# Optimization experiments

Hardware: AMD Instinct MI355X
Metric: run time of the kernel (lower is better)

The kernel has to match this reference:

```python
import jax, jax.numpy as jnp
import numpy as np

BSZ, SEQ, HID = 8, 4096, 1024
N_EXPERTS = 8
CAPACITY = 512  # expert_capacity_per_batch; effective cap = min(SEQ, CAPACITY)
SCALE = 1.0     # routed_scaling_factor


def setup_inputs() -> dict:
    key = jax.random.key(0)
    k1, k2 = jax.random.split(key)
    hidden_states = jax.random.normal(k1, (BSZ, SEQ, HID), dtype=jnp.float32)
    # kaiming_uniform_(a=sqrt(5)) on [d,e] -> bound = 1/sqrt(fan_in=d)
    bound = 1.0 / np.sqrt(HID)
    weight = jax.random.uniform(k2, (HID, N_EXPERTS), dtype=jnp.float32,
                                minval=-bound, maxval=bound)
    return {"hidden_states": hidden_states, "weight": weight}


def reference(hidden_states, weight):
    bsz, seq_len, h = hidden_states.shape
    # gating logits in fp32: [b, s, e]
    logits = jnp.einsum('bsd,de->bse', hidden_states.astype(jnp.float32),
                        weight.astype(jnp.float32))
    affinity = jax.nn.softmax(logits, axis=-1)          # [b, s, e]
    affinity = jnp.transpose(affinity, (0, 2, 1))       # [b, e, s]
    cap = min(seq_len, CAPACITY)                        # static
    # Each expert picks its top-`cap` tokens (sorted descending, like torch.topk)
    topk_scores, topk_indices = jax.lax.top_k(affinity, cap)  # [b, e, cap]
    topk_scores = topk_scores * SCALE
    # dense dispatch mask [b, e, cap, s]: one-hot over token positions
    dispatch_mask = jax.nn.one_hot(topk_indices, seq_len, dtype=jnp.float32)
    return topk_indices, topk_scores, dispatch_mask
```

## Files before the change

kernel.cpp:

```cpp
#include <hip/hip_runtime.h>

constexpr int BSZ = 8, SEQ = 4096, HID = 1024, NE = 8, CAP = 512;
constexpr int ROWS = BSZ * NE;
constexpr size_t IDX_ELEMS = (size_t)ROWS * CAP;
constexpr size_t SCR_OFF = IDX_ELEMS;
constexpr size_t MASK_OFF = IDX_ELEMS * 2;
constexpr size_t MASK_ELEMS = (size_t)ROWS * CAP * SEQ;
constexpr size_t AFF_ELEMS = (size_t)ROWS * SEQ;

typedef float f4v __attribute__((ext_vector_type(4)));

__global__ __launch_bounds__(128) void gating_kernel(const float* __restrict__ hidden,
                                                     const float* __restrict__ weight,
                                                     float* __restrict__ aff)
{
    __shared__ float hls[16][68];
    __shared__ float wls[8][68];
    __shared__ float lls[16][8];

    const int tid = threadIdx.x;
    const int T0 = blockIdx.x * 16;
    const int t = tid >> 3;
    const int e = tid & 7;

    float v0 = 0.f, v1 = 0.f, v2 = 0.f, v3 = 0.f;
    for (int c = 0; c < 16; ++c) {
        __syncthreads();
#pragma unroll
        for (int k = 0; k < 2; ++k) {
            const int j = tid + k * 128;
            const int tt = j >> 4, q = j & 15;
            const float4 v = *(const float4*)(hidden + (size_t)(T0 + tt) * HID + c * 64 + 4 * q);
            *(float4*)&hls[tt][4 * q] = v;
        }
#pragma unroll
        for (int k = 0; k < 4; ++k) {
            const int j = tid + k * 128;
            const int dd = j >> 3, ee = j & 7;
            wls[ee][dd] = weight[(size_t)(c * 64 + dd) * NE + ee];
        }
        __syncthreads();
#pragma unroll
        for (int k = 0; k < 4; ++k) {
            const int base = 16 * k;
            const float4 hA = *(const float4*)&hls[t][base + 0];
            const float4 hB = *(const float4*)&hls[t][base + 4];
            const float4 hC = *(const float4*)&hls[t][base + 8];
            const float4 hD = *(const float4*)&hls[t][base + 12];
            const float4 wA = *(const float4*)&wls[e][base + 0];
            const float4 wB = *(const float4*)&wls[e][base + 4];
            const float4 wC = *(const float4*)&wls[e][base + 8];
            const float4 wD = *(const float4*)&wls[e][base + 12];
            v0 = __fadd_rn(__fmul_rn(hA.x, wA.x),
                 __fadd_rn(__fmul_rn(hB.x, wB.x),
                 __fadd_rn(__fmul_rn(hC.x, wC.x),
                 __fadd_rn(__fmul_rn(hD.x, wD.x), v0))));
            v1 = __fadd_rn(__fmul_rn(hA.y, wA.y),
                 __fadd_rn(__fmul_rn(hB.y, wB.y),
                 __fadd_rn(__fmul_rn(hC.y, wC.y),
                 __fadd_rn(__fmul_rn(hD.y, wD.y), v1))));
            v2 = __fadd_rn(__fmul_rn(hA.z, wA.z),
                 __fadd_rn(__fmul_rn(hB.z, wB.z),
                 __fadd_rn(__fmul_rn(hC.z, wC.z),
                 __fadd_rn(__fmul_rn(hD.z, wD.z), v2))));
            v3 = __fadd_rn(__fmul_rn(hA.w, wA.w),
                 __fadd_rn(__fmul_rn(hB.w, wB.w),
                 __fadd_rn(__fmul_rn(hC.w, wC.w),
                 __fadd_rn(__fmul_rn(hD.w, wD.w), v3))));
        }
    }
    const float logit = __fadd_rn(__fadd_rn(v0, v1), __fadd_rn(v2, v3));

    lls[t][e] = logit;
    __syncthreads();

    float l[8];
#pragma unroll
    for (int k = 0; k < 8; ++k) l[k] = lls[t][k];
    float m = l[0];
#pragma unroll
    for (int k = 1; k < 8; ++k) m = fmaxf(m, l[k]);
    float p[8];
#pragma unroll
    for (int k = 0; k < 8; ++k)
        p[k] = (float)exp((double)__fsub_rn(l[k], m));
    const float s = __fadd_rn(__fadd_rn(__fadd_rn(p[0], p[1]), __fadd_rn(p[2], p[3])),
                              __fadd_rn(__fadd_rn(p[4], p[5]), __fadd_rn(p[6], p[7])));
    const float a = __fdiv_rn(p[e], s);

    const int token = T0 + t;
    const int b = token >> 12;
    const int sidx = token & (SEQ - 1);
    aff[((size_t)b * NE + e) * SEQ + sidx] = a;
}

__global__ __launch_bounds__(1024) void topk_zero_kernel(const float* __restrict__ aff,
                                                         float* __restrict__ out,
                                                         long long zero_elems)
{
    __shared__ unsigned long long keys[SEQ];
    if (blockIdx.x < (unsigned)ROWS) {
        const int row = blockIdx.x;
        const float* a = aff + (size_t)row * SEQ;
        for (int i = threadIdx.x; i < SEQ; i += 1024) {
            const unsigned int fb = __float_as_uint(a[i]);
            keys[i] = ((unsigned long long)fb << 32) | (unsigned int)(SEQ - 1 - i);
        }
        for (int len = 2; len <= SEQ; len <<= 1) {
            for (int stride = len >> 1; stride > 0; stride >>= 1) {
                __syncthreads();
                for (int t = threadIdx.x; t < SEQ / 2; t += 1024) {
                    const int i = (t << 1) - (t & (stride - 1));
                    const int j = i + stride;
                    const unsigned long long ki = keys[i], kj = keys[j];
                    const bool desc = ((i & len) == 0);
                    if (desc ? (ki < kj) : (ki > kj)) { keys[i] = kj; keys[j] = ki; }
                }
            }
        }
        __syncthreads();
        if (threadIdx.x < CAP) {
            const int t = threadIdx.x;
            const unsigned long long k = keys[t];
            const int idx = (SEQ - 1) - (int)(unsigned int)(k & 0xffffffffu);
            out[(size_t)row * CAP + t] = (float)idx;
            out[SCR_OFF + (size_t)row * CAP + t] =
                __uint_as_float((unsigned int)(k >> 32));
        }
    } else {
        const long long nz4 = zero_elems >> 2;
        f4v* mz = (f4v*)(out + MASK_OFF);
        const f4v z4 = {0.f, 0.f, 0.f, 0.f};
        const long long stride = (long long)(gridDim.x - ROWS) * 1024;
        for (long long i = (long long)(blockIdx.x - ROWS) * 1024 + threadIdx.x;
             i < nz4; i += stride)
            __builtin_nontemporal_store(z4, mz + i);
    }
}

__global__ void tailzero_kernel(float* __restrict__ out)
{
    const long long n4 = (long long)(AFF_ELEMS >> 2);
    f4v* mz = (f4v*)(out + MASK_OFF + MASK_ELEMS - AFF_ELEMS);
    const f4v z4 = {0.f, 0.f, 0.f, 0.f};
    const long long i = (long long)blockIdx.x * blockDim.x + threadIdx.x;
    if (i < n4) __builtin_nontemporal_store(z4, mz + i);
}

__global__ void scatter_kernel(float* __restrict__ out)
{
    const int p = blockIdx.x * blockDim.x + threadIdx.x;
    if (p < (int)IDX_ELEMS) {
        const int idx = (int)out[p];
        out[MASK_OFF + (size_t)p * SEQ + idx] = 1.0f;
    }
}

extern "C" void kernel_launch(void* const* d_in, const int* in_sizes, int n_in,
                              void* d_out, int out_size, void* d_ws, size_t ws_size,
                              hipStream_t stream)
{
    const float* hidden = (const float*)d_in[0];
    const float* weight = (const float*)d_in[1];
    float* out = (float*)d_out;

    const bool use_ws = (ws_size >= AFF_ELEMS * sizeof(float));
    float* aff = use_ws ? (float*)d_ws
                        : (out + MASK_OFF + MASK_ELEMS - AFF_ELEMS);

    gating_kernel<<<2048, 128, 0, stream>>>(hidden, weight, aff);

    const long long zero_elems = use_ws ? (long long)MASK_ELEMS
                                        : (long long)(MASK_ELEMS - AFF_ELEMS);
    topk_zero_kernel<<<ROWS + 1984, 1024, 0, stream>>>(aff, out, zero_elems);

    if (!use_ws)
        tailzero_kernel<<<256, 256, 0, stream>>>(out);

    scatter_kernel<<<(int)((IDX_ELEMS + 255) / 256), 256, 0, stream>>>(out);
}
```

Baseline: 654.4 us.

## Fuse mask zeroing and one-hot scatter into per-row bitonic sort kernel

When a workspace is available, a new kernel runs one block per (batch, expert) row. Each block sorts the row and interleaves nontemporal zero stores for that row's slice of the dispatch mask between sort stages, then writes the one-hot 1.0 entries directly. This removes the separate scatter kernel and the extra launch, and hides zeroing behind the sort's shared-memory work. The trade-off is that the full mask clear is now issued by only 64 blocks instead of about 2000, so HBM may not be saturated. It also relies on the zero stores and the later 1.0 stores from the same block landing in order.

```diff
diff --git a/kernel.cpp b/kernel.cpp
--- a/kernel.cpp
+++ b/kernel.cpp
@@ -94,6 +94,54 @@
     aff[((size_t)b * NE + e) * SEQ + sidx] = a;
 }
 
+__global__ __launch_bounds__(1024) void sortzero_kernel(const float* __restrict__ aff,
+                                                        float* __restrict__ out)
+{
+    __shared__ unsigned long long keys[SEQ];
+    const int row = blockIdx.x;
+    const float* a = aff + (size_t)row * SEQ;
+    float* mrow = out + MASK_OFF + (size_t)row * CAP * SEQ;
+
+    for (int i = threadIdx.x; i < SEQ; i += 1024) {
+        const unsigned int fb = __float_as_uint(a[i]);
+        keys[i] = ((unsigned long long)fb << 32) | (unsigned int)(SEQ - 1 - i);
+    }
+
+    f4v* mz = (f4v*)mrow;
+    const f4v z4 = {0.f, 0.f, 0.f, 0.f};
+    int zi = 0;
+
+    for (int len = 2; len <= SEQ; len <<= 1) {
+        for (int stride = len >> 1; stride > 0; stride >>= 1) {
+            __syncthreads();
+#pragma unroll
+            for (int k = 0; k < 7; ++k) {
+                if (zi < 512) {
+                    __builtin_nontemporal_store(z4, mz + (size_t)zi * 1024 + threadIdx.x);
+                    ++zi;
+                }
+            }
+            for (int t = threadIdx.x; t < SEQ / 2; t += 1024) {
+                const int i = (t << 1) - (t & (stride - 1));
+                const int j = i + stride;
+                const unsigned long long ki = keys[i], kj = keys[j];
+                const bool desc = ((i & len) == 0);
+                if (desc ? (ki < kj) : (ki > kj)) { keys[i] = kj; keys[j] = ki; }
+            }
+        }
+    }
+    __syncthreads();
+    if (threadIdx.x < CAP) {
+        const int t = threadIdx.x;
+        const unsigned long long k = keys[t];
+        const int idx = (SEQ - 1) - (int)(unsigned int)(k & 0xffffffffu);
+        out[(size_t)row * CAP + t] = (float)idx;
+        out[SCR_OFF + (size_t)row * CAP + t] =
+            __uint_as_float((unsigned int)(k >> 32));
+        mrow[(size_t)t * SEQ + idx] = 1.0f;
+    }
+}
+
 __global__ __launch_bounds__(1024) void topk_zero_kernel(const float* __restrict__ aff,
                                                          float* __restrict__ out,
                                                          long long zero_elems)
@@ -165,17 +213,17 @@
     float* out = (float*)d_out;
 
     const bool use_ws = (ws_size >= AFF_ELEMS * sizeof(float));
-    float* aff = use_ws ? (float*)d_ws
-                        : (out + MASK_OFF + MASK_ELEMS - AFF_ELEMS);
-
-    gating_kernel<<<2048, 128, 0, stream>>>(hidden, weight, aff);
-
-    const long long zero_elems = use_ws ? (long long)MASK_ELEMS
-                                        : (long long)(MASK_ELEMS - AFF_ELEMS);
-    topk_zero_kernel<<<ROWS + 1984, 1024, 0, stream>>>(aff, out, zero_elems);
-
-    if (!use_ws)
+
+    if (use_ws) {
+        float* aff = (float*)d_ws;
+        gating_kernel<<<2048, 128, 0, stream>>>(hidden, weight, aff);
+        sortzero_kernel<<<ROWS, 1024, 0, stream>>>(aff, out);
+    } else {
+        float* aff = out + MASK_OFF + MASK_ELEMS - AFF_ELEMS;
+        gating_kernel<<<2048, 128, 0, stream>>>(hidden, weight, aff);
+        const long long zero_elems = (long long)(MASK_ELEMS - AFF_ELEMS);
+        topk_zero_kernel<<<ROWS + 1984, 1024, 0, stream>>>(aff, out, zero_elems);
         tailzero_kernel<<<256, 256, 0, stream>>>(out);
-
-    scatter_kernel<<<(int)((IDX_ELEMS + 255) / 256), 256, 0, stream>>>(out);
-}
+        scatter_kernel<<<(int)((IDX_ELEMS + 255) / 256), 256, 0, stream>>>(out);
+    }
+}
```

New measurement: 640.0 us. 2.2% less time.
